# Optimization experiments

Hardware: AMD Instinct MI355X
Metric: run time of the kernel (lower is better)

## Reference

```python
import jax, jax.numpy as jnp
import numpy as np

CP_SPACING = (4, 4, 4)
SIGMAS = tuple(0.44 * cp for cp in CP_SPACING)


def _gaussian_kernel_3d(sigmas):
    # Faithful to DeepReg layer_util.gaussian_filter_3d
    ks = [int(np.ceil(s * 3) + np.mod(np.ceil(s * 3) + 1, 2)) for s in sigmas]
    grid = np.stack(np.meshgrid(*[np.arange(k) for k in ks], indexing="ij"), axis=0)  # [3,k,k,k]
    mean = ((np.asarray(ks, np.float64) - 1.0) / 2.0).reshape(-1, 1, 1, 1)
    var = (np.asarray(sigmas, np.float64) ** 2.0).reshape(-1, 1, 1, 1)
    norm = 1.0 / (np.sqrt(2.0 * np.pi) ** 3 + np.prod(sigmas))  # as in DeepReg source
    kernel = norm * np.exp(-np.sum((grid - mean) ** 2.0 / (2.0 * var), axis=0))
    kernel = kernel / np.sum(kernel)  # sums to 1
    return kernel.astype(np.float32)  # [k,k,k]


def setup_inputs() -> dict:
    key = jax.random.key(0)
    image = jax.random.normal(key, (4, 160, 160, 160, 3), dtype=jnp.float32)  # DDF volume, 3 channels
    kernel = jnp.asarray(_gaussian_kernel_3d(SIGMAS))  # deterministic [7,7,7] Gaussian buffer
    return {"image": image, "kernel": kernel}


def reference(image, kernel):
    b, d1, d2, d3, c = image.shape
    # DeepReg's [k,k,k,3,3] diagonal kernel == depthwise blur per channel.
    kdw = jnp.tile(kernel[..., None, None], (1, 1, 1, 1, c))  # [k,k,k,1,C]
    blurred = jax.lax.conv_general_dilated(
        image, kdw,
        window_strides=(1, 1, 1),
        padding="SAME",
        dimension_numbers=("NDHWC", "DHWIO", "NDHWC"),
        feature_group_count=c,
    )
    # output control-point grid: ceil(dim / cp_spacing) + 3
    size = tuple(int(np.ceil(v / cp)) + 3 for v, cp in zip((d1, d2, d3), CP_SPACING))
    # tf.image.resize bilinear (TF2) uses half-pixel centers == jax.image.resize 'linear'
    out = jax.image.resize(blurred, (b,) + size + (c,), method="linear")
    return out
```

## Files before the change

kernel.cpp:

```cpp
#include <hip/hip_runtime.h>
#include <hip/hip_fp16.h>

#define NB 4
#define NI 160
#define NO 43
#define NC 3
#define KS 7
#define KPAD 3
#define MT 16
#define CH 8
#define CH1 4
#define P1B 128
#define NP 22

#define ROWF (NI * NC)
#define PROW 132
#define PROW4 (PROW / 4)
#define LROW 484
#define SLICE (NO * NO * NC)

#define A1H_BYTES ((size_t)NB * NI * NI * PROW * 2)
#define A2_BYTES  ((size_t)NB * NI * NO * PROW * 4)
#define P2_THREADS ((size_t)NB * NI * NO * PROW4)
#define P3_THREADS ((size_t)NB * NO * NO * PROW4)

struct __align__(16) Tables {
    float wa3[NO][20];
    float w1[NO][MT];
    float wp[NP][24][2];
    int   o1h[NO][MT];
    int   o0[NO][MT];
    int   j3[NO];
    int   jlo[NO];
};

constexpr double ctaylor(double r) {
    double s = 1.0, term = 1.0;
    for (int n = 1; n <= 13; ++n) { term *= r / (double)n; s += term; }
    return s;
}
constexpr double cexp_neg(double x) {
    double y = -x;
    int k = (int)(y * 16.0);
    double r = y - (double)k / 16.0;
    double e16 = ctaylor(1.0 / 16.0);
    double p = 1.0;
    for (int i = 0; i < k; ++i) p *= e16;
    return 1.0 / (p * ctaylor(r));
}
constexpr int cceil(double x)  { int c = (int)x; return ((double)c < x) ? c + 1 : c; }
constexpr int cfloor(double x) { int f = (int)x; return ((double)f > x) ? f - 1 : f; }
constexpr double cabsd(double x) { return x < 0 ? -x : x; }

constexpr double comp_w(int j, double sf, int ilo, int ihi, const double* g) {
    if (j >= NI || j < 0) return 0.0;
    double cw = 0.0;
    for (int t = 0; t < KS; ++t) {
        int i = j + KPAD - t;
        if (i >= ilo && i <= ihi) {
            double w = 1.0 - cabsd(sf - (double)i) * (43.0 / 160.0);
            if (w > 0.0) cw += g[t] * w;
        }
    }
    return cw;
}

struct Band { double sf; int ilo; int ihi; double wsum; };
constexpr Band bandof(int o) {
    const double inv_scale = 160.0 / 43.0;
    double sf = ((double)o + 0.5) * inv_scale - 0.5;
    int ilo = cceil(sf - inv_scale);  if (ilo < 0) ilo = 0;
    int ihi = cfloor(sf + inv_scale); if (ihi > NI - 1) ihi = NI - 1;
    double wsum = 0.0;
    for (int i = ilo; i <= ihi; ++i) {
        double w = 1.0 - cabsd(sf - (double)i) * (43.0 / 160.0);
        if (w > 0.0) wsum += w;
    }
    return {sf, ilo, ihi, wsum};
}

constexpr Tables make_tables() {
    Tables T{};
    double g[KS] = {};
    double gs = 0.0;
    const double sig = 0.44 * 4.0;
    for (int i = 0; i < KS; ++i) {
        double d = (double)i - 3.0;
        g[i] = cexp_neg(-(d * d) / (2.0 * sig * sig));
        gs += g[i];
    }
    for (int i = 0; i < KS; ++i) g[i] /= gs;

    for (int o = 0; o < NO; ++o) {
        Band B = bandof(o);
        int jlo = B.ilo - KPAD; if (jlo < 0) jlo = 0;
        int j0 = jlo & ~3;
        T.j3[o] = j0;
        T.jlo[o] = jlo;
        for (int m = 0; m < 20; ++m)
            T.wa3[o][m] = (float)(comp_w(j0 + m, B.sf, B.ilo, B.ihi, g) / B.wsum);
        for (int k = 0; k < MT; ++k) {
            int j = jlo + k;
            T.w1[o][k] = (float)(comp_w(j, B.sf, B.ilo, B.ihi, g) / B.wsum);
            int jc = (j < NI) ? j : (NI - 1);
            T.o1h[o][k] = jc * (PROW * 2);
            T.o0[o][k]  = jc * (NO * PROW * 4);
        }
    }
    for (int p = 0; p < NP; ++p) {
        int oA = 2 * p, oB = 2 * p + 1;
        Band BA = bandof(oA);
        int jp = T.j3[oA];
        for (int k = 0; k < 24; ++k) {
            T.wp[p][k][0] = (float)(comp_w(jp + k, BA.sf, BA.ilo, BA.ihi, g) / BA.wsum);
            if (oB < NO) {
                Band BB = bandof(oB);
                T.wp[p][k][1] = (float)(comp_w(jp + k, BB.sf, BB.ilo, BB.ihi, g) / BB.wsum);
            } else {
                T.wp[p][k][1] = 0.0f;
            }
        }
    }
    return T;
}

__constant__ Tables dT = make_tables();

struct __align__(8) h4 { __half2 lo, hi; };
union h2u { __half2 h; unsigned int u; };

__global__ __launch_bounds__(P1B) void k_p1(
        const float* __restrict__ img, __half* __restrict__ A1h) {
    __shared__ __align__(16) float rows[CH1 * LROW + 64];
    int t = threadIdx.x;
    int blk = blockIdx.x;

    const int p = t % NP, row = t / NP;
    const bool has = (t < NP * CH1);

    float4 wq0, wq1, wq2, wq3, wq4, wq5, wq6, wq7, wq8, wq9, wq10, wq11;
    int jp = 0;
    if (has) {
        jp = dT.j3[2 * p];
        const float4* wpp = (const float4*)dT.wp[p];
        wq0 = wpp[0];  wq1 = wpp[1];  wq2 = wpp[2];  wq3 = wpp[3];
        wq4 = wpp[4];  wq5 = wpp[5];  wq6 = wpp[6];  wq7 = wpp[7];
        wq8 = wpp[8];  wq9 = wpp[9];  wq10 = wpp[10]; wq11 = wpp[11];
    }

    const float4* src = (const float4*)(img + (size_t)blk * (CH1 * ROWF));
    for (int g = t; g < CH1 * ROWF / 4; g += P1B) {
        int r = g / 120, m = g % 120;
        *(float4*)(rows + r * LROW + 4 * m) = src[g];
    }
    if (t < 16) rows[(t >> 2) * LROW + ROWF + (t & 3)] = 0.f;
    if (t >= 16 && t < 80) rows[CH1 * LROW + (t - 16)] = 0.f;
    __syncthreads();

    if (has) {
        const float4* dp = (const float4*)(rows + row * LROW + 3 * jp);
        float a0 = 0.f, a1 = 0.f, a2 = 0.f;
        float b0 = 0.f, b1 = 0.f, b2 = 0.f;
#define STEP(M, WQA, WQB) {                                                    \
            float4 v0 = dp[3*(M)], v1 = dp[3*(M)+1], v2 = dp[3*(M)+2];         \
            a0 += WQA.x * v0.x; a1 += WQA.x * v0.y; a2 += WQA.x * v0.z;        \
            b0 += WQA.y * v0.x; b1 += WQA.y * v0.y; b2 += WQA.y * v0.z;        \
            a0 += WQA.z * v0.w; a1 += WQA.z * v1.x; a2 += WQA.z * v1.y;        \
            b0 += WQA.w * v0.w; b1 += WQA.w * v1.x; b2 += WQA.w * v1.y;        \
            a0 += WQB.x * v1.z; a1 += WQB.x * v1.w; a2 += WQB.x * v2.x;        \
            b0 += WQB.y * v1.z; b1 += WQB.y * v1.w; b2 += WQB.y * v2.x;        \
            a0 += WQB.z * v2.y; a1 += WQB.z * v2.z; a2 += WQB.z * v2.w;        \
            b0 += WQB.w * v2.y; b1 += WQB.w * v2.z; b2 += WQB.w * v2.w;        \
        }
        STEP(0, wq0, wq1)  STEP(1, wq2, wq3)  STEP(2, wq4, wq5)
        STEP(3, wq6, wq7)  STEP(4, wq8, wq9)  STEP(5, wq10, wq11)
#undef STEP
        h2u c0, c1, c2;
        c0.h = __floats2half2_rn(a0, a1);
        c1.h = __floats2half2_rn(a2, b0);
        c2.h = __floats2half2_rn(b1, b2);
        unsigned int* dstu = (unsigned int*)A1h;
        size_t baseu = ((size_t)blk * CH1 + row) * (PROW / 2) + 3 * p;
        dstu[baseu] = c0.u; dstu[baseu + 1] = c1.u; dstu[baseu + 2] = c2.u;
    }
}

__device__ __forceinline__ int xcd_swz(int wg, int nwg) {
    int q = nwg >> 3, r = nwg & 7;
    int x = wg & 7, i = wg >> 3;
    return (x < r ? x * (q + 1) : r * (q + 1) + (x - r) * q) + i;
}

__global__ __launch_bounds__(256) void k_p2(
        const __half* __restrict__ A1h, float* __restrict__ A2) {
    int blk = xcd_swz(blockIdx.x, gridDim.x);
    size_t idx = (size_t)blk * 256 + threadIdx.x;
    if (idx >= P2_THREADS) return;
    int ii = (int)idx;
    int col4 = ii % PROW4;
    int o2   = (ii / PROW4) % NO;
    int slab = ii / (PROW4 * NO);
    const char* base = (const char*)A1h + ((size_t)slab * NI * PROW + col4 * 4) * 2;
    const float4* wv = (const float4*)dT.w1[o2];
    const int4*   ov = (const int4*)dT.o1h[o2];
    float4 w0 = wv[0], w1v = wv[1], w2 = wv[2], w3 = wv[3];
    int4   j0 = ov[0], j1 = ov[1], j2 = ov[2], j3 = ov[3];
    float4 a = {0.f, 0.f, 0.f, 0.f};
#define TAP4H(J, W) { h4 v = *(const h4*)(base + (unsigned)(J));               \
                      float2 f0 = __half22float2(v.lo);                        \
                      float2 f1 = __half22float2(v.hi);                        \
                      a.x += (W) * f0.x; a.y += (W) * f0.y;                    \
                      a.z += (W) * f1.x; a.w += (W) * f1.y; }
    TAP4H(j0.x, w0.x) TAP4H(j0.y, w0.y) TAP4H(j0.z, w0.z) TAP4H(j0.w, w0.w)
    TAP4H(j1.x, w1v.x) TAP4H(j1.y, w1v.y) TAP4H(j1.z, w1v.z) TAP4H(j1.w, w1v.w)
    TAP4H(j2.x, w2.x) TAP4H(j2.y, w2.y) TAP4H(j2.z, w2.z) TAP4H(j2.w, w2.w)
    TAP4H(j3.x, w3.x) TAP4H(j3.y, w3.y) TAP4H(j3.z, w3.z) TAP4H(j3.w, w3.w)
#undef TAP4H
    ((float4*)A2)[idx] = a;
}

__global__ __launch_bounds__(256) void k_p3(
        const float* __restrict__ A2, float* __restrict__ out) {
    int blk = xcd_swz(blockIdx.x, gridDim.x);
    size_t idx = (size_t)blk * 256 + threadIdx.x;
    if (idx >= P3_THREADS) return;
    int ii = (int)idx;
    int col4 = ii % PROW4;
    int o2   = (ii / PROW4) % NO;
    int o1   = (ii / (PROW4 * NO)) % NO;
    int b    = ii / (PROW4 * NO * NO);
    const char* base = (const char*)A2 +
        (((size_t)b * NI * NO + o2) * PROW + col4 * 4) * 4;
    const float4* wv = (const float4*)dT.w1[o1];
    const int4*   ov = (const int4*)dT.o0[o1];
    float4 w0 = wv[0], w1v = wv[1], w2 = wv[2], w3 = wv[3];
    int4   j0 = ov[0], j1 = ov[1], j2 = ov[2], j3 = ov[3];
    float4 a = {0.f, 0.f, 0.f, 0.f};
#define TAP4(J, W) { float4 v = *(const float4*)(base + (unsigned)(J)); \
                     a.x += (W) * v.x; a.y += (W) * v.y; a.z += (W) * v.z; a.w += (W) * v.w; }
    TAP4(j0.x, w0.x) TAP4(j0.y, w0.y) TAP4(j0.z, w0.z) TAP4(j0.w, w0.w)
    TAP4(j1.x, w1v.x) TAP4(j1.y, w1v.y) TAP4(j1.z, w1v.z) TAP4(j1.w, w1v.w)
    TAP4(j2.x, w2.x) TAP4(j2.y, w2.y) TAP4(j2.z, w2.z) TAP4(j2.w, w2.w)
    TAP4(j3.x, w3.x) TAP4(j3.y, w3.y) TAP4(j3.z, w3.z) TAP4(j3.w, w3.w)
#undef TAP4
    int tile = (b * NO + o1) * NO + o2;
    float* ob = out + (size_t)tile * (NO * NC) + col4 * 4;
    int col = col4 * 4;
    float av[4] = {a.x, a.y, a.z, a.w};
    #pragma unroll
    for (int e = 0; e < 4; ++e)
        if (col + e < NO * NC) ob[e] = av[e];
}

__global__ __launch_bounds__(256) void k_passA(
        const float* __restrict__ img, float* __restrict__ S) {
    __shared__ float rows[CH * NI * NC];
    __shared__ float T[CH * NO * NC];
    __shared__ float acc[NO * NO * NC];
    __shared__ float w2[NO * MT];
    __shared__ int   s2[NO];
    int t = threadIdx.x;
    int blk = blockIdx.x;
    const float* src = img + (size_t)blk * (NI * NI * NC);
    for (int k = t; k < NO * MT; k += 256) w2[k] = ((const float*)dT.w1)[k];
    for (int k = t; k < NO; k += 256) s2[k] = dT.jlo[k];
    for (int k = t; k < NO * NO * NC; k += 256) acc[k] = 0.f;
    __syncthreads();
    for (int chunk = 0; chunk < NI / CH; ++chunk) {
        const float4* csrc = (const float4*)(src + (size_t)chunk * CH * NI * NC);
        for (int k = t; k < CH * NI * NC / 4; k += 256)
            ((float4*)rows)[k] = csrc[k];
        __syncthreads();
        for (int task = t; task < CH * NO; task += 256) {
            int ch = task / NO, o3 = task % NO;
            int st = s2[o3];
            const float* rp = rows + ch * NI * NC;
            float a0 = 0.f, a1 = 0.f, a2 = 0.f;
            #pragma unroll
            for (int k = 0; k < MT; ++k) {
                int j = st + k; j = (j < NI) ? j : (NI - 1);
                float w = w2[o3 * MT + k];
                a0 += w * rp[j * 3 + 0];
                a1 += w * rp[j * 3 + 1];
                a2 += w * rp[j * 3 + 2];
            }
            T[task * NC + 0] = a0;
            T[task * NC + 1] = a1;
            T[task * NC + 2] = a2;
        }
        __syncthreads();
        int i2base = chunk * CH;
        for (int task = t; task < NO * NO; task += 256) {
            int o2 = task / NO, o3 = task % NO;
            int st = s2[o2];
            int k0 = i2base - st;        k0 = (k0 > 0) ? k0 : 0;
            int k1 = i2base + CH - st;   k1 = (k1 < MT) ? k1 : MT;
            if (k1 > k0) {
                float a0 = 0.f, a1 = 0.f, a2 = 0.f;
                for (int k = k0; k < k1; ++k) {
                    float w = w2[o2 * MT + k];
                    int ch = st + k - i2base;
                    a0 += w * T[(ch * NO + o3) * NC + 0];
                    a1 += w * T[(ch * NO + o3) * NC + 1];
                    a2 += w * T[(ch * NO + o3) * NC + 2];
                }
                acc[task * NC + 0] += a0;
                acc[task * NC + 1] += a1;
                acc[task * NC + 2] += a2;
            }
        }
        __syncthreads();
    }
    float* Sp = S + (size_t)blk * (NO * NO * NC);
    for (int k = t; k < NO * NO * NC; k += 256) Sp[k] = acc[k];
}

__global__ __launch_bounds__(256) void k_passB(
        const float* __restrict__ S, float* __restrict__ out) {
    int blk = blockIdx.x;
    int b = blk / NO, o1 = blk % NO;
    __shared__ float w1s[MT];
    __shared__ int s1v;
    if (threadIdx.x < MT) w1s[threadIdx.x] = dT.w1[o1][threadIdx.x];
    if (threadIdx.x == 0) s1v = dT.jlo[o1];
    __syncthreads();
    const float* Sb = S + (size_t)b * NI * (NO * NO * NC);
    float* ob = out + (size_t)blk * (NO * NO * NC);
    int st = s1v;
    for (int e = threadIdx.x; e < NO * NO * NC; e += 256) {
        float a = 0.f;
        #pragma unroll
        for (int k = 0; k < MT; ++k) {
            int i1 = st + k; i1 = (i1 < NI) ? i1 : (NI - 1);
            a += w1s[k] * Sb[(size_t)i1 * (NO * NO * NC) + e];
        }
        ob[e] = a;
    }
}

extern "C" void kernel_launch(void* const* d_in, const int* in_sizes, int n_in,
                              void* d_out, int out_size, void* d_ws, size_t ws_size,
                              hipStream_t stream) {
    (void)in_sizes; (void)n_in; (void)out_size;
    const float* img = (const float*)d_in[0];
    float* out = (float*)d_out;
    char* ws = (char*)d_ws;

    if (ws_size >= A1H_BYTES + A2_BYTES) {
        __half* A1h = (__half*)ws;
        float*  A2  = (float*)(ws + A1H_BYTES);
        k_p1<<<NB * NI * (NI / CH1), P1B, 0, stream>>>(img, A1h);
        int p2b = (int)((P2_THREADS + 255) / 256);
        k_p2<<<p2b, 256, 0, stream>>>(A1h, A2);
        int p3b = (int)((P3_THREADS + 255) / 256);
        k_p3<<<p3b, 256, 0, stream>>>(A2, out);
    } else {
        float* S = (float*)ws;
        k_passA<<<NB * NI, 256, 0, stream>>>(img, S);
        k_passB<<<NB * NO, 256, 0, stream>>>(S, out);
    }
}
```

Before: 69.37 us.

## Store second-pass intermediate in fp16 and compute output pairs per thread

The second-axis pass now has each thread compute two adjacent output positions over a shared 24-tap window using paired weight tables, which halves the thread count and reuses the loaded input taps. The intermediate volume A2 is stored in half precision instead of float, halving its write and read traffic, and the third pass reads it through fp16 offset tables. This trades extra precision loss in the intermediate and more registers per thread for less memory traffic and fewer loads.

```diff
diff --git a/kernel.cpp b/kernel.cpp
--- a/kernel.cpp
+++ b/kernel.cpp
@@ -20,16 +20,15 @@
 #define SLICE (NO * NO * NC)
 
 #define A1H_BYTES ((size_t)NB * NI * NI * PROW * 2)
-#define A2_BYTES  ((size_t)NB * NI * NO * PROW * 4)
-#define P2_THREADS ((size_t)NB * NI * NO * PROW4)
+#define A2H_BYTES ((size_t)NB * NI * NO * PROW * 2)
+#define P2P_THREADS ((size_t)NB * NI * NP * PROW4)
 #define P3_THREADS ((size_t)NB * NO * NO * PROW4)
 
 struct __align__(16) Tables {
-    float wa3[NO][20];
     float w1[NO][MT];
     float wp[NP][24][2];
-    int   o1h[NO][MT];
-    int   o0[NO][MT];
+    int   o1hp[NP][24];
+    int   o0h[NO][MT];
     int   j3[NO];
     int   jlo[NO];
 };
@@ -94,17 +93,13 @@
     for (int o = 0; o < NO; ++o) {
         Band B = bandof(o);
         int jlo = B.ilo - KPAD; if (jlo < 0) jlo = 0;
-        int j0 = jlo & ~3;
-        T.j3[o] = j0;
+        T.j3[o] = jlo & ~3;
         T.jlo[o] = jlo;
-        for (int m = 0; m < 20; ++m)
-            T.wa3[o][m] = (float)(comp_w(j0 + m, B.sf, B.ilo, B.ihi, g) / B.wsum);
         for (int k = 0; k < MT; ++k) {
             int j = jlo + k;
             T.w1[o][k] = (float)(comp_w(j, B.sf, B.ilo, B.ihi, g) / B.wsum);
             int jc = (j < NI) ? j : (NI - 1);
-            T.o1h[o][k] = jc * (PROW * 2);
-            T.o0[o][k]  = jc * (NO * PROW * 4);
+            T.o0h[o][k] = jc * (NO * PROW * 2);
         }
     }
     for (int p = 0; p < NP; ++p) {
@@ -119,6 +114,8 @@
             } else {
                 T.wp[p][k][1] = 0.0f;
             }
+            int jc = (jp + k < NI) ? (jp + k) : (NI - 1);
+            T.o1hp[p][k] = jc * (PROW * 2);
         }
     }
     return T;
@@ -192,17 +189,65 @@
 }
 
 __global__ __launch_bounds__(256) void k_p2(
-        const __half* __restrict__ A1h, float* __restrict__ A2) {
+        const __half* __restrict__ A1h, __half* __restrict__ A2h) {
     int blk = xcd_swz(blockIdx.x, gridDim.x);
     size_t idx = (size_t)blk * 256 + threadIdx.x;
-    if (idx >= P2_THREADS) return;
+    if (idx >= P2P_THREADS) return;
+    int ii = (int)idx;
+    int col4 = ii % PROW4;
+    int p    = (ii / PROW4) % NP;
+    int slab = ii / (PROW4 * NP);
+    const char* base = (const char*)A1h + ((size_t)slab * NI * PROW + col4 * 4) * 2;
+    const float4* wpp = (const float4*)dT.wp[p];
+    const int4*   ot  = (const int4*)dT.o1hp[p];
+    float4 wq0 = wpp[0], wq1 = wpp[1], wq2 = wpp[2],  wq3 = wpp[3];
+    float4 wq4 = wpp[4], wq5 = wpp[5], wq6 = wpp[6],  wq7 = wpp[7];
+    float4 wq8 = wpp[8], wq9 = wpp[9], wq10 = wpp[10], wq11 = wpp[11];
+    int4 t0 = ot[0], t1 = ot[1], t2 = ot[2], t3 = ot[3], t4 = ot[4], t5 = ot[5];
+    float4 a = {0.f,0.f,0.f,0.f}, b = a;
+#define TP(J, WA, WB) { h4 v = *(const h4*)(base + (unsigned)(J));             \
+        float2 f0 = __half22float2(v.lo), f1 = __half22float2(v.hi);           \
+        a.x += (WA) * f0.x; a.y += (WA) * f0.y;                                \
+        a.z += (WA) * f1.x; a.w += (WA) * f1.y;                                \
+        b.x += (WB) * f0.x; b.y += (WB) * f0.y;                                \
+        b.z += (WB) * f1.x; b.w += (WB) * f1.y; }
+    TP(t0.x, wq0.x, wq0.y)  TP(t0.y, wq0.z, wq0.w)
+    TP(t0.z, wq1.x, wq1.y)  TP(t0.w, wq1.z, wq1.w)
+    TP(t1.x, wq2.x, wq2.y)  TP(t1.y, wq2.z, wq2.w)
+    TP(t1.z, wq3.x, wq3.y)  TP(t1.w, wq3.z, wq3.w)
+    TP(t2.x, wq4.x, wq4.y)  TP(t2.y, wq4.z, wq4.w)
+    TP(t2.z, wq5.x, wq5.y)  TP(t2.w, wq5.z, wq5.w)
+    TP(t3.x, wq6.x, wq6.y)  TP(t3.y, wq6.z, wq6.w)
+    TP(t3.z, wq7.x, wq7.y)  TP(t3.w, wq7.z, wq7.w)
+    TP(t4.x, wq8.x, wq8.y)  TP(t4.y, wq8.z, wq8.w)
+    TP(t4.z, wq9.x, wq9.y)  TP(t4.w, wq9.z, wq9.w)
+    TP(t5.x, wq10.x, wq10.y) TP(t5.y, wq10.z, wq10.w)
+    TP(t5.z, wq11.x, wq11.y) TP(t5.w, wq11.z, wq11.w)
+#undef TP
+    h4* A2h4 = (h4*)A2h;
+    size_t rbase = ((size_t)slab * NO + 2 * p) * PROW4 + col4;
+    h4 ra; ra.lo = __floats2half2_rn(a.x, a.y); ra.hi = __floats2half2_rn(a.z, a.w);
+    A2h4[rbase] = ra;
+    if (2 * p + 1 < NO) {
+        h4 rb; rb.lo = __floats2half2_rn(b.x, b.y); rb.hi = __floats2half2_rn(b.z, b.w);
+        A2h4[rbase + PROW4] = rb;
+    }
+}
+
+__global__ __launch_bounds__(256) void k_p3(
+        const __half* __restrict__ A2h, float* __restrict__ out) {
+    int blk = xcd_swz(blockIdx.x, gridDim.x);
+    size_t idx = (size_t)blk * 256 + threadIdx.x;
+    if (idx >= P3_THREADS) return;
     int ii = (int)idx;
     int col4 = ii % PROW4;
     int o2   = (ii / PROW4) % NO;
-    int slab = ii / (PROW4 * NO);
-    const char* base = (const char*)A1h + ((size_t)slab * NI * PROW + col4 * 4) * 2;
-    const float4* wv = (const float4*)dT.w1[o2];
-    const int4*   ov = (const int4*)dT.o1h[o2];
+    int o1   = (ii / (PROW4 * NO)) % NO;
+    int b    = ii / (PROW4 * NO * NO);
+    const char* base = (const char*)A2h +
+        (((size_t)b * NI * NO + o2) * PROW + col4 * 4) * 2;
+    const float4* wv = (const float4*)dT.w1[o1];
+    const int4*   ov = (const int4*)dT.o0h[o1];
     float4 w0 = wv[0], w1v = wv[1], w2 = wv[2], w3 = wv[3];
     int4   j0 = ov[0], j1 = ov[1], j2 = ov[2], j3 = ov[3];
     float4 a = {0.f, 0.f, 0.f, 0.f};
@@ -216,33 +261,6 @@
     TAP4H(j2.x, w2.x) TAP4H(j2.y, w2.y) TAP4H(j2.z, w2.z) TAP4H(j2.w, w2.w)
     TAP4H(j3.x, w3.x) TAP4H(j3.y, w3.y) TAP4H(j3.z, w3.z) TAP4H(j3.w, w3.w)
 #undef TAP4H
-    ((float4*)A2)[idx] = a;
-}
-
-__global__ __launch_bounds__(256) void k_p3(
-        const float* __restrict__ A2, float* __restrict__ out) {
-    int blk = xcd_swz(blockIdx.x, gridDim.x);
-    size_t idx = (size_t)blk * 256 + threadIdx.x;
-    if (idx >= P3_THREADS) return;
-    int ii = (int)idx;
-    int col4 = ii % PROW4;
-    int o2   = (ii / PROW4) % NO;
-    int o1   = (ii / (PROW4 * NO)) % NO;
-    int b    = ii / (PROW4 * NO * NO);
-    const char* base = (const char*)A2 +
-        (((size_t)b * NI * NO + o2) * PROW + col4 * 4) * 4;
-    const float4* wv = (const float4*)dT.w1[o1];
-    const int4*   ov = (const int4*)dT.o0[o1];
-    float4 w0 = wv[0], w1v = wv[1], w2 = wv[2], w3 = wv[3];
-    int4   j0 = ov[0], j1 = ov[1], j2 = ov[2], j3 = ov[3];
-    float4 a = {0.f, 0.f, 0.f, 0.f};
-#define TAP4(J, W) { float4 v = *(const float4*)(base + (unsigned)(J)); \
-                     a.x += (W) * v.x; a.y += (W) * v.y; a.z += (W) * v.z; a.w += (W) * v.w; }
-    TAP4(j0.x, w0.x) TAP4(j0.y, w0.y) TAP4(j0.z, w0.z) TAP4(j0.w, w0.w)
-    TAP4(j1.x, w1v.x) TAP4(j1.y, w1v.y) TAP4(j1.z, w1v.z) TAP4(j1.w, w1v.w)
-    TAP4(j2.x, w2.x) TAP4(j2.y, w2.y) TAP4(j2.z, w2.z) TAP4(j2.w, w2.w)
-    TAP4(j3.x, w3.x) TAP4(j3.y, w3.y) TAP4(j3.z, w3.z) TAP4(j3.w, w3.w)
-#undef TAP4
     int tile = (b * NO + o1) * NO + o2;
     float* ob = out + (size_t)tile * (NO * NC) + col4 * 4;
     int col = col4 * 4;
@@ -346,14 +364,14 @@
     float* out = (float*)d_out;
     char* ws = (char*)d_ws;
 
-    if (ws_size >= A1H_BYTES + A2_BYTES) {
+    if (ws_size >= A1H_BYTES + A2H_BYTES) {
         __half* A1h = (__half*)ws;
-        float*  A2  = (float*)(ws + A1H_BYTES);
+        __half* A2h = (__half*)(ws + A1H_BYTES);
         k_p1<<<NB * NI * (NI / CH1), P1B, 0, stream>>>(img, A1h);
-        int p2b = (int)((P2_THREADS + 255) / 256);
-        k_p2<<<p2b, 256, 0, stream>>>(A1h, A2);
+        int p2b = (int)((P2P_THREADS + 255) / 256);
+        k_p2<<<p2b, 256, 0, stream>>>(A1h, A2h);
         int p3b = (int)((P3_THREADS + 255) / 256);
-        k_p3<<<p3b, 256, 0, stream>>>(A2, out);
+        k_p3<<<p3b, 256, 0, stream>>>(A2h, out);
     } else {
         float* S = (float*)ws;
         k_passA<<<NB * NI, 256, 0, stream>>>(img, S);
```

Result: faster. 67.47 us (-2.7%).
